# Kernel tuning notes

Hardware: AMD Instinct MI355X
Metric: run time of the kernel (lower is better)

## Reference

```python
import jax, jax.numpy as jnp
import numpy as np

N = 50000          # masked node count
E = 800000         # edges (avg degree 16)
IN_DIM, GCN_DIM, REL_DIM, TRAIN_DIM, OUT_DIM = 3, 128, 64, 128, 2
BATCHES = 1


def setup_inputs() -> dict:
    key = jax.random.key(0)
    ks = jax.random.split(key, 16)
    s = 0.05
    return {
        "features": jax.random.normal(ks[0], (N, IN_DIM), jnp.float32),
        "edge_index": jax.random.randint(ks[1], (2, E), 0, N, dtype=jnp.int32),
        "trainOT": jax.random.normal(ks[2], (TRAIN_DIM,), jnp.float32),
        "W1": jax.random.normal(ks[3], (IN_DIM, GCN_DIM), jnp.float32) * s,
        "b1": jnp.zeros((GCN_DIM,), jnp.float32),
        "W2": jax.random.normal(ks[4], (GCN_DIM, GCN_DIM), jnp.float32) * s,
        "b2": jnp.zeros((GCN_DIM,), jnp.float32),
        "Wq": jax.random.normal(ks[5], (GCN_DIM, REL_DIM), jnp.float32) * s,
        "bq": jnp.zeros((REL_DIM,), jnp.float32),
        "Wk": jax.random.normal(ks[6], (TRAIN_DIM, REL_DIM), jnp.float32) * s,
        "bk": jnp.zeros((REL_DIM,), jnp.float32),
        "Wv": jax.random.normal(ks[7], (GCN_DIM, TRAIN_DIM), jnp.float32) * s,
        "bv": jnp.zeros((TRAIN_DIM,), jnp.float32),
        "Ws": jax.random.normal(ks[8], (TRAIN_DIM, OUT_DIM * N), jnp.float32) * s,
        "bs": jnp.zeros((OUT_DIM * N,), jnp.float32),
    }


def _gcn_conv(x, W, b, src, dst, n):
    """PyG GCNConv: h = D^-1/2 (A+I) D^-1/2 (x W) + b (self-loops already in src/dst)."""
    h = x @ W                                                  # [n, d_out]
    ones = jnp.ones(src.shape[0], dtype=x.dtype)
    deg = jax.ops.segment_sum(ones, dst, num_segments=n)      # in-degree incl. self-loop
    dinv = jnp.where(deg > 0, jax.lax.rsqrt(deg), 0.0)
    norm = dinv[src] * dinv[dst]                               # [E+n]
    msg = h[src] * norm[:, None]                               # gather (dominant traffic)
    return jax.ops.segment_sum(msg, dst, num_segments=n) + b   # scatter-add


def reference(features, edge_index, trainOT, W1, b1, W2, b2, Wq, bq, Wk, bk, Wv, bv, Ws, bs):
    n = features.shape[0]
    loop = jnp.arange(n, dtype=edge_index.dtype)
    src = jnp.concatenate([edge_index[0], loop])
    dst = jnp.concatenate([edge_index[1], loop])

    h1 = jax.nn.relu(_gcn_conv(features, W1, b1, src, dst, n))   # gcn1 + relu
    h2 = _gcn_conv(h1, W2, b2, src, dst, n)                      # gcn2

    q = h2 @ Wq + bq                                             # [n, rel]
    v = h2 @ Wv + bv                                             # [n, train]
    k = trainOT @ Wk + bk                                        # [rel]
    scale = jnp.asarray(Wq.shape[1], q.dtype) ** 0.5
    rel = jax.nn.sigmoid((q @ k) / scale)                        # [n]
    summed_idea = (rel[:, None] * v).sum(axis=0)                 # [train]
    new_trainOT = trainOT + summed_idea
    speak = new_trainOT @ Ws + bs                                # [out_dim * num_nodes]
    out = speak.reshape(BATCHES, -1, OUT_DIM)
    return out, new_trainOT
```

## Files before the change

### kernel.cpp

```cpp
#include <hip/hip_runtime.h>
#include <math.h>

#define O_RPD    (0)
#define O_DINV   (512*1024)
#define O_SMALL  (768*1024)
#define O_Y      (1024*1024)
#define O_RELW   (1280*1024)
#define O_REL    (1536*1024)
#define O_GHD    (1792*1024)
#define O_GHS    (2048*1024)
#define O_GOD    (2304*1024)
#define O_GOS    (2560*1024)
#define O_BSD    (2816*1024)
#define O_BSS    (2944*1024)
#define O_PART   (3072*1024)
#define O_XS     (3712*1024)
#define O_G1     (4608*1024)
#define O_SRTD   (5632*1024)
#define O_SRTS   (9216*1024)
#define O_COLD   (12544*1024)

#define NCHUNK 256

static __device__ __forceinline__ int blockExclScan256(int v, volatile int* lds, int t) {
    int lane = t & 63, wid = t >> 6;
    int incl = v;
#pragma unroll
    for (int off = 1; off < 64; off <<= 1) {
        int n = __shfl_up(incl, off);
        if (lane >= off) incl += n;
    }
    if (lane == 63) lds[wid] = incl;
    __syncthreads();
    if (t == 0) {
        int s = 0;
#pragma unroll
        for (int i = 0; i < 4; ++i) { int x = lds[i]; lds[i] = s; s += x; }
    }
    __syncthreads();
    return lds[wid] + incl - v;
}

__global__ void k_hist(const int* __restrict__ eidx, int* __restrict__ ghD,
                       int* __restrict__ ghS,
                       const float* __restrict__ trainOT, const float* __restrict__ Wq,
                       const float* __restrict__ bq, const float* __restrict__ Wk,
                       const float* __restrict__ bk, const float* __restrict__ W2,
                       const float* __restrict__ b2, float* __restrict__ small,
                       int E, int CS, int NB) {
    int b = blockIdx.x, t = threadIdx.x;
    if (b == NCHUNK) {
        if (blockIdx.y) return;
        __shared__ float kv[64];
        __shared__ float wqk[128];
        __shared__ float fred[256];
        if (t < 64) {
            float acc = bk[t];
            for (int j = 0; j < 128; ++j) acc += trainOT[j] * Wk[j * 64 + t];
            kv[t] = acc;
        }
        __syncthreads();
        if (t < 128) {
            float aq = 0.f;
            for (int c2 = 0; c2 < 64; ++c2) aq += Wq[t * 64 + c2] * kv[c2];
            wqk[t] = aq;
        }
        fred[t] = (t < 64) ? bq[t] * kv[t] : 0.f;
        __syncthreads();
        for (int off = 128; off >= 1; off >>= 1) { if (t < off) fred[t] += fred[t + off]; __syncthreads(); }
        float bqs = fred[0];
        __syncthreads();
        if (t < 128) {
            float a2 = 0.f;
            for (int j = 0; j < 128; ++j) a2 += W2[t * 128 + j] * wqk[j];
            small[t] = a2;
        }
        fred[t] = (t < 128) ? b2[t] * wqk[t] : 0.f;
        __syncthreads();
        for (int off = 128; off >= 1; off >>= 1) { if (t < off) fred[t] += fred[t + off]; __syncthreads(); }
        if (t == 0) small[128] = bqs + fred[0];
        return;
    }
    __shared__ int lh[256];
    const int* arr = blockIdx.y ? eidx : (eidx + E);
    int* gh = blockIdx.y ? ghS : ghD;
    lh[t] = 0; __syncthreads();
    int s = b * CS, e = min(E, s + CS);
    for (int i = s + t; i < e; i += 256) atomicAdd(&lh[arr[i] >> 8], 1);
    __syncthreads();
    if (t < NB) gh[t * NCHUNK + b] = lh[t];
}

__global__ void k_goff(const int* __restrict__ ghD, const int* __restrict__ ghS,
                       int* __restrict__ goD, int* __restrict__ goS,
                       int* __restrict__ bsD, int* __restrict__ bsS, int E, int NB) {
    __shared__ int lred[256];
    __shared__ int lds1[4];
    int nb = blockIdx.x, t = threadIdx.x;
    const int* gh = blockIdx.y ? ghS : ghD;
    int* go = blockIdx.y ? goS : goD;
    int* bs = blockIdx.y ? bsS : bsD;
    int rs = 0;
    if (t < nb) {
        const int4* row = reinterpret_cast<const int4*>(gh + t * NCHUNK);
        for (int i = 0; i < NCHUNK / 4; ++i) { int4 p = row[i]; rs += p.x + p.y + p.z + p.w; }
    }
    lred[t] = rs; __syncthreads();
    for (int off = 128; off >= 1; off >>= 1) { if (t < off) lred[t] += lred[t + off]; __syncthreads(); }
    int base = lred[0];
    __syncthreads();
    if (t == 0) { bs[nb] = base; if (nb == NB - 1) bs[NB] = E; }
    int g = gh[nb * NCHUNK + t];
    int gx = blockExclScan256(g, lds1, t);
    go[nb * NCHUNK + t] = base + gx;
}

__global__ void k_scatter(const int* __restrict__ eidx, const int* __restrict__ goD,
                          const int* __restrict__ goS, unsigned int* __restrict__ srtD,
                          unsigned int* __restrict__ srtS, int E, int CS, int NB) {
    __shared__ int lcur[256];
    int b = blockIdx.x, t = threadIdx.x;
    const int* key = blockIdx.y ? eidx : (eidx + E);
    const int* val = blockIdx.y ? (eidx + E) : eidx;
    const int* go  = blockIdx.y ? goS : goD;
    unsigned int* srt = blockIdx.y ? srtS : srtD;
    if (t < NB) lcur[t] = go[t * NCHUNK + b];
    __syncthreads();
    int s = b * CS, e = min(E, s + CS);
    for (int i = s + t; i < e; i += 256) {
        int k = key[i];
        int pos = atomicAdd(&lcur[k >> 8], 1);
        srt[pos] = ((unsigned int)(k & 255) << 16) | (unsigned int)val[i];
    }
}

__global__ void k_build(const unsigned int* __restrict__ srtD, const int* __restrict__ bsD,
                        int* __restrict__ rpD, int* __restrict__ colD,
                        float* __restrict__ dinv, const float* __restrict__ x,
                        float4* __restrict__ xs4, int N) {
    __shared__ int lcnt[256];
    __shared__ int lpos[256];
    __shared__ int lds1[4];
    int nb = blockIdx.x, t = threadIdx.x;
    lcnt[t] = 0; __syncthreads();
    int s = bsD[nb], e = bsD[nb + 1];
    for (int i = s + t; i < e; i += 256) atomicAdd(&lcnt[srtD[i] >> 16], 1);
    __syncthreads();
    int c = lcnt[t];
    int cx = blockExclScan256(c, lds1, t);
    int rpv = s + cx;
    int node = (nb << 8) + t;
    rpD[node] = rpv;
    lpos[t] = rpv;
    if (node < N) {
        float d = rsqrtf((float)(c + 1));
        dinv[node] = d;
        float4 v;
        v.x = x[node * 3] * d; v.y = x[node * 3 + 1] * d; v.z = x[node * 3 + 2] * d; v.w = 0.f;
        xs4[node] = v;
    }
    __syncthreads();
    for (int i = s + t; i < e; i += 256) {
        unsigned int v = srtD[i];
        int p = atomicAdd(&lpos[v >> 16], 1);
        colD[p] = (int)(v & 0xffffu);
    }
}

__global__ void k_y(const float4* __restrict__ xs4, const int* __restrict__ rpD,
                    const int* __restrict__ colD, const float* __restrict__ dinv,
                    const float* __restrict__ W1, const float* __restrict__ b1,
                    const float* __restrict__ small, float4* __restrict__ g1,
                    float* __restrict__ y, int N) {
    int t = threadIdx.x;
    int sub = t & 15;
    int node = blockIdx.x * 16 + (t >> 4);
    if (node >= N) return;
    float di = dinv[node];
    int s = rpD[node], e = rpD[node + 1];
    float a0 = 0.f, a1 = 0.f, a2 = 0.f;
    for (int j = s + sub; j < e; j += 16) {
        float4 xv = xs4[colD[j]];
        a0 += xv.x; a1 += xv.y; a2 += xv.z;
    }
    if (sub == 0) { float4 xv = xs4[node]; a0 += xv.x; a1 += xv.y; a2 += xv.z; }
#pragma unroll
    for (int off = 1; off < 16; off <<= 1) {
        a0 += __shfl_xor(a0, off);
        a1 += __shfl_xor(a1, off);
        a2 += __shfl_xor(a2, off);
    }
    a0 *= di; a1 *= di; a2 *= di;
    float yl = 0.f;
#pragma unroll
    for (int m = 0; m < 8; ++m) {
        int c = sub * 8 + m;
        float h = fmaxf(a0 * W1[c] + a1 * W1[128 + c] + a2 * W1[256 + c] + b1[c], 0.f);
        yl += h * small[c];
    }
#pragma unroll
    for (int off = 1; off < 16; off <<= 1) yl += __shfl_xor(yl, off);
    if (sub == 0) {
        y[node] = yl * di;
        float4 gv; gv.x = a0; gv.y = a1; gv.z = a2; gv.w = di;
        g1[node] = gv;
    }
}

__global__ void k_dv(const float* __restrict__ y, const int* __restrict__ rpD,
                     const int* __restrict__ colD, const float* __restrict__ dinv,
                     const float* __restrict__ small, float* __restrict__ relw,
                     float* __restrict__ rel, int N) {
    int t = threadIdx.x;
    int sub = t & 15;
    int node = blockIdx.x * 16 + (t >> 4);
    if (node >= N) return;
    float di = dinv[node];
    int s = rpD[node], e = rpD[node + 1];
    float acc = (sub == 0) ? y[node] : 0.f;
    for (int j = s + sub; j < e; j += 16) acc += y[colD[j]];
#pragma unroll
    for (int off = 1; off < 16; off <<= 1) acc += __shfl_xor(acc, off);
    float z = (acc * di + small[128]) * 0.125f;
    float r = 1.f / (1.f + __expf(-z));
    if (sub == 0) { rel[node] = r; relw[node] = r * di; }
}

__global__ void k_zS(const unsigned int* __restrict__ srtS, const int* __restrict__ bsS,
                     const float* __restrict__ relw, const float* __restrict__ rel,
                     const float4* __restrict__ g1, const float* __restrict__ W1,
                     const float* __restrict__ b1, float* __restrict__ part, int N) {
    __shared__ float zl[256];
    __shared__ float W1s[384];
    __shared__ float b1s[128];
    __shared__ float sS[4][132];
    int nb = blockIdx.x, t = threadIdx.x, lane = t & 63, wid = t >> 6;
    int sub = lane & 15, gid = wid * 4 + (lane >> 4);
    int node0 = (nb << 8) + t;
    zl[t] = (node0 < N) ? relw[node0] : 0.f;
    if (t < 128) { W1s[t] = W1[t]; W1s[128 + t] = W1[128 + t]; W1s[256 + t] = W1[256 + t];
                   b1s[t] = b1[t]; }
    __syncthreads();
    int s = bsS[nb], e = bsS[nb + 1];
    for (int i = s + t; i < e; i += 256) {
        unsigned int v = srtS[i];
        atomicAdd(&zl[v >> 16], relw[v & 0xffffu]);
    }
    __syncthreads();
    float sacc[8];
#pragma unroll
    for (int m = 0; m < 8; ++m) sacc[m] = 0.f;
    float Racc = 0.f;
#pragma unroll 4
    for (int r = 0; r < 16; ++r) {
        int nl = gid * 16 + r;
        int node = (nb << 8) + nl;
        if (node < N) {
            float4 gv = g1[node];
            float zw = zl[nl] * gv.w;
#pragma unroll
            for (int m = 0; m < 8; ++m) {
                int c = sub * 8 + m;
                float h = fmaxf(gv.x * W1s[c] + gv.y * W1s[128 + c] + gv.z * W1s[256 + c] + b1s[c], 0.f);
                sacc[m] += zw * h;
            }
            if (sub == 0) Racc += rel[node];
        }
    }
#pragma unroll
    for (int m = 0; m < 8; ++m) {
        sacc[m] += __shfl_xor(sacc[m], 16);
        sacc[m] += __shfl_xor(sacc[m], 32);
    }
    Racc += __shfl_xor(Racc, 16);
    Racc += __shfl_xor(Racc, 32);
    if (lane < 16) {
#pragma unroll
        for (int m = 0; m < 8; ++m) sS[wid][sub * 8 + m] = sacc[m];
    }
    if (lane == 0) sS[wid][128] = Racc;
    __syncthreads();
    if (t < 129) part[t * 256 + nb] = sS[0][t] + sS[1][t] + sS[2][t] + sS[3][t];
}

__global__ void k_speak(const float* __restrict__ Ws, const float* __restrict__ bs,
                        const float* __restrict__ trainOT, const float* __restrict__ W2,
                        const float* __restrict__ b2, const float* __restrict__ Wv,
                        const float* __restrict__ bv, const float* __restrict__ part,
                        float* __restrict__ out, int out_n, int NB) {
    __shared__ float Ss[129];
    __shared__ float t1[128];
    __shared__ float nt[128];
    __shared__ float s0[256], s1[256];
    int t = threadIdx.x;
    if (t < 129) {
        const float4* p4 = reinterpret_cast<const float4*>(part + t * 256);
        float a = 0.f;
        int n4 = NB >> 2;
        for (int i = 0; i < n4; ++i) { float4 v = p4[i]; a += v.x + v.y + v.z + v.w; }
        for (int i = n4 << 2; i < NB; ++i) a += part[t * 256 + i];
        Ss[t] = a;
    }
    __syncthreads();
    float R = Ss[128];
    if (t < 128) {
        float a = R * b2[t];
        for (int j = 0; j < 128; ++j) a += Ss[j] * W2[j * 128 + t];
        t1[t] = a;
    }
    __syncthreads();
    if (t < 128) {
        float a = R * bv[t];
        for (int j = 0; j < 128; ++j) a += t1[j] * Wv[j * 128 + t];
        float v = trainOT[t] + a;
        nt[t] = v;
        if (blockIdx.x == 0) out[out_n + t] = v;
    }
    __syncthreads();
    int jj = (t & 63) * 2, sl = t >> 6;
    int j = blockIdx.x * 128 + jj;
    float a0 = 0.f, a1 = 0.f;
    if (j < out_n) {
        const float* w = Ws + (size_t)(sl * 32) * out_n + j;
        for (int k = 0; k < 32; ++k) {
            float cv = nt[sl * 32 + k];
            float2 r = *reinterpret_cast<const float2*>(w + (size_t)k * out_n);
            a0 += cv * r.x; a1 += cv * r.y;
        }
    }
    s0[t] = a0; s1[t] = a1; __syncthreads();
    if (t < 64 && j < out_n) {
        out[j]     = s0[t] + s0[t + 64] + s0[t + 128] + s0[t + 192] + bs[j];
        out[j + 1] = s1[t] + s1[t + 64] + s1[t + 128] + s1[t + 192] + bs[j + 1];
    }
}

extern "C" void kernel_launch(void* const* d_in, const int* in_sizes, int n_in,
                              void* d_out, int out_size, void* d_ws, size_t ws_size,
                              hipStream_t stream) {
    const float* features = (const float*)d_in[0];
    const int*   eidx     = (const int*)d_in[1];
    const float* trainOT  = (const float*)d_in[2];
    const float* W1 = (const float*)d_in[3];
    const float* b1 = (const float*)d_in[4];
    const float* W2 = (const float*)d_in[5];
    const float* b2 = (const float*)d_in[6];
    const float* Wq = (const float*)d_in[7];
    const float* bq = (const float*)d_in[8];
    const float* Wk = (const float*)d_in[9];
    const float* bk = (const float*)d_in[10];
    const float* Wv = (const float*)d_in[11];
    const float* bv = (const float*)d_in[12];
    const float* Ws = (const float*)d_in[13];
    const float* bs = (const float*)d_in[14];

    int N = in_sizes[0] / 3;
    int E = in_sizes[1] / 2;
    int NB = (N + 255) >> 8;
    int CS = (E + NCHUNK - 1) / NCHUNK;

    char* ws = (char*)d_ws;
    int*   rpD   = (int*)(ws + O_RPD);
    float* dinv  = (float*)(ws + O_DINV);
    float* small = (float*)(ws + O_SMALL);
    float* y     = (float*)(ws + O_Y);
    float* relw  = (float*)(ws + O_RELW);
    float* rel   = (float*)(ws + O_REL);
    int*   ghD   = (int*)(ws + O_GHD);
    int*   ghS   = (int*)(ws + O_GHS);
    int*   goD   = (int*)(ws + O_GOD);
    int*   goS   = (int*)(ws + O_GOS);
    int*   bsD   = (int*)(ws + O_BSD);
    int*   bsS   = (int*)(ws + O_BSS);
    float* part  = (float*)(ws + O_PART);
    float4* xs4  = (float4*)(ws + O_XS);
    float4* g1   = (float4*)(ws + O_G1);
    unsigned int* srtD = (unsigned int*)(ws + O_SRTD);
    unsigned int* srtS = (unsigned int*)(ws + O_SRTS);
    int*   colD  = (int*)(ws + O_COLD);
    float* out   = (float*)d_out;
    int out_n = out_size - 128;

    k_hist<<<dim3(NCHUNK + 1, 2), 256, 0, stream>>>(eidx, ghD, ghS,
                                                    trainOT, Wq, bq, Wk, bk, W2, b2, small,
                                                    E, CS, NB);
    k_goff<<<dim3(NB, 2), 256, 0, stream>>>(ghD, ghS, goD, goS, bsD, bsS, E, NB);
    k_scatter<<<dim3(NCHUNK, 2), 256, 0, stream>>>(eidx, goD, goS, srtD, srtS, E, CS, NB);
    k_build<<<NB, 256, 0, stream>>>(srtD, bsD, rpD, colD, dinv, features, xs4, N);
    k_y<<<(N + 15) / 16, 256, 0, stream>>>(xs4, rpD, colD, dinv, W1, b1, small, g1, y, N);
    k_dv<<<(N + 15) / 16, 256, 0, stream>>>(y, rpD, colD, dinv, small, relw, rel, N);
    k_zS<<<NB, 256, 0, stream>>>(srtS, bsS, relw, rel, g1, W1, b1, part, N);
    k_speak<<<(out_n + 127) / 128, 256, 0, stream>>>(Ws, bs, trainOT, W2, b2, Wv, bv,
                                                     part, out, out_n, NB);
}
```

Measured before the change: 109.2 us.

## Compute new trainOT once in last k_zS block instead of per k_speak block

Before this change, every k_speak block (about 782 of them) re-reduced the partial sums and redid the two 128x128 matvecs (W2, Wv) before its slice of the Ws product. Now the last k_zS block to finish, found through an atomic counter with thread fences, does this once, splits each matvec over 256 threads, and writes new_trainOT to workspace and to the output tail. k_speak only reads the 128-vector. This adds a serial tail step in one block and counter/fence overhead. It relies on the counter being reset in k_hist.

Result: slower. 121.2 us (+11.0%).

```diff
diff --git a/kernel.cpp b/kernel.cpp
--- a/kernel.cpp
+++ b/kernel.cpp
@@ -47,13 +47,14 @@
                        const float* __restrict__ bq, const float* __restrict__ Wk,
                        const float* __restrict__ bk, const float* __restrict__ W2,
                        const float* __restrict__ b2, float* __restrict__ small,
-                       int E, int CS, int NB) {
+                       unsigned int* __restrict__ counter, int E, int CS, int NB) {
     int b = blockIdx.x, t = threadIdx.x;
     if (b == NCHUNK) {
         if (blockIdx.y) return;
         __shared__ float kv[64];
         __shared__ float wqk[128];
         __shared__ float fred[256];
+        if (t == 0) counter[0] = 0u;
         if (t < 64) {
             float acc = bk[t];
             for (int j = 0; j < 128; ++j) acc += trainOT[j] * Wk[j * 64 + t];
@@ -229,7 +230,12 @@
 __global__ void k_zS(const unsigned int* __restrict__ srtS, const int* __restrict__ bsS,
                      const float* __restrict__ relw, const float* __restrict__ rel,
                      const float4* __restrict__ g1, const float* __restrict__ W1,
-                     const float* __restrict__ b1, float* __restrict__ part, int N) {
+                     const float* __restrict__ b1, float* __restrict__ part,
+                     const float* __restrict__ trainOT, const float* __restrict__ W2,
+                     const float* __restrict__ b2, const float* __restrict__ Wv,
+                     const float* __restrict__ bv, float* __restrict__ small,
+                     unsigned int* __restrict__ counter, float* __restrict__ out_tail,
+                     int N, int NB) {
     __shared__ float zl[256];
     __shared__ float W1s[384];
     __shared__ float b1s[128];
@@ -281,18 +287,16 @@
     if (lane == 0) sS[wid][128] = Racc;
     __syncthreads();
     if (t < 129) part[t * 256 + nb] = sS[0][t] + sS[1][t] + sS[2][t] + sS[3][t];
-}
-
-__global__ void k_speak(const float* __restrict__ Ws, const float* __restrict__ bs,
-                        const float* __restrict__ trainOT, const float* __restrict__ W2,
-                        const float* __restrict__ b2, const float* __restrict__ Wv,
-                        const float* __restrict__ bv, const float* __restrict__ part,
-                        float* __restrict__ out, int out_n, int NB) {
+    __threadfence();
+    __syncthreads();
+    __shared__ unsigned int lastFlag;
+    if (t == 0) lastFlag = (atomicAdd(counter, 1u) == (unsigned int)(NB - 1)) ? 1u : 0u;
+    __syncthreads();
+    if (!lastFlag) return;
+    __threadfence();
     __shared__ float Ss[129];
-    __shared__ float t1[128];
-    __shared__ float nt[128];
-    __shared__ float s0[256], s1[256];
-    int t = threadIdx.x;
+    __shared__ float t1s[128];
+    __shared__ float red2[256];
     if (t < 129) {
         const float4* p4 = reinterpret_cast<const float4*>(part + t * 256);
         float a = 0.f;
@@ -303,19 +307,28 @@
     }
     __syncthreads();
     float R = Ss[128];
+    int o = t & 127, sl2 = t >> 7;
+    float a1 = 0.f;
+    for (int j = sl2 * 64; j < sl2 * 64 + 64; ++j) a1 += Ss[j] * W2[j * 128 + o];
+    red2[t] = a1; __syncthreads();
+    if (t < 128) t1s[t] = R * b2[t] + red2[t] + red2[t + 128];
+    __syncthreads();
+    float a2 = 0.f;
+    for (int j = sl2 * 64; j < sl2 * 64 + 64; ++j) a2 += t1s[j] * Wv[j * 128 + o];
+    red2[t] = a2; __syncthreads();
     if (t < 128) {
-        float a = R * b2[t];
-        for (int j = 0; j < 128; ++j) a += Ss[j] * W2[j * 128 + t];
-        t1[t] = a;
-    }
-    __syncthreads();
-    if (t < 128) {
-        float a = R * bv[t];
-        for (int j = 0; j < 128; ++j) a += t1[j] * Wv[j * 128 + t];
-        float v = trainOT[t] + a;
-        nt[t] = v;
-        if (blockIdx.x == 0) out[out_n + t] = v;
-    }
+        float nt = trainOT[t] + R * bv[t] + red2[t] + red2[t + 128];
+        small[264 + t] = nt;
+        out_tail[t] = nt;
+    }
+}
+
+__global__ void k_speak(const float* __restrict__ Ws, const float* __restrict__ bs,
+                        const float* __restrict__ small, float* __restrict__ out, int out_n) {
+    __shared__ float nt[128];
+    __shared__ float s0[256], s1[256];
+    int t = threadIdx.x;
+    if (t < 128) nt[t] = small[264 + t];
     __syncthreads();
     int jj = (t & 63) * 2, sl = t >> 6;
     int j = blockIdx.x * 128 + jj;
@@ -363,6 +376,7 @@
     int*   rpD   = (int*)(ws + O_RPD);
     float* dinv  = (float*)(ws + O_DINV);
     float* small = (float*)(ws + O_SMALL);
+    unsigned int* counter = (unsigned int*)(ws + O_SMALL + 2048);
     float* y     = (float*)(ws + O_Y);
     float* relw  = (float*)(ws + O_RELW);
     float* rel   = (float*)(ws + O_REL);
@@ -383,13 +397,13 @@
 
     k_hist<<<dim3(NCHUNK + 1, 2), 256, 0, stream>>>(eidx, ghD, ghS,
                                                     trainOT, Wq, bq, Wk, bk, W2, b2, small,
-                                                    E, CS, NB);
+                                                    counter, E, CS, NB);
     k_goff<<<dim3(NB, 2), 256, 0, stream>>>(ghD, ghS, goD, goS, bsD, bsS, E, NB);
     k_scatter<<<dim3(NCHUNK, 2), 256, 0, stream>>>(eidx, goD, goS, srtD, srtS, E, CS, NB);
     k_build<<<NB, 256, 0, stream>>>(srtD, bsD, rpD, colD, dinv, features, xs4, N);
     k_y<<<(N + 15) / 16, 256, 0, stream>>>(xs4, rpD, colD, dinv, W1, b1, small, g1, y, N);
     k_dv<<<(N + 15) / 16, 256, 0, stream>>>(y, rpD, colD, dinv, small, relw, rel, N);
-    k_zS<<<NB, 256, 0, stream>>>(srtS, bsS, relw, rel, g1, W1, b1, part, N);
-    k_speak<<<(out_n + 127) / 128, 256, 0, stream>>>(Ws, bs, trainOT, W2, b2, Wv, bv,
-                                                     part, out, out_n, NB);
-}
+    k_zS<<<NB, 256, 0, stream>>>(srtS, bsS, relw, rel, g1, W1, b1, part,
+                                 trainOT, W2, b2, Wv, bv, small, counter, out + out_n, N, NB);
+    k_speak<<<(out_n + 127) / 128, 256, 0, stream>>>(Ws, bs, small, out, out_n);
+}
```
